# Optimization experiments

Measured on AMD Instinct MI355X. Metric: run time of the kernel, lower is better.

The kernel has to match this reference:

```python
import jax, jax.numpy as jnp
import numpy as np

N = 262144      # active voxels
K = 27          # 3^3 kernel offsets
C_IN = 64
C_OUT = 64
EPS = 1e-5      # BatchNorm eps (torch default)


def setup_inputs() -> dict:
    key = jax.random.key(0)
    k1, k2, k3, k4, k5 = jax.random.split(key, 5)
    features = jax.random.normal(k1, (N, C_IN), dtype=jnp.float32)
    # kernel map: for each offset k and output point i, index of the input
    # neighbor; value == N means 'no neighbor' (maps to a zero pad row)
    nbr_idx = jax.random.randint(k2, (K, N), 0, N + 1)
    weight = jax.random.normal(k3, (K, C_IN, C_OUT), dtype=jnp.float32) * (1.0 / np.sqrt(K * C_IN))
    gamma = jax.random.uniform(k4, (C_OUT,), dtype=jnp.float32, minval=0.5, maxval=1.5)
    beta = jax.random.normal(k5, (C_OUT,), dtype=jnp.float32) * 0.1
    return {"features": features, "nbr_idx": nbr_idx, "weight": weight,
            "gamma": gamma, "beta": beta}


def reference(features, nbr_idx, weight, gamma, beta):
    # zero pad row so idx == N contributes nothing (missing neighbor)
    padded = jnp.concatenate(
        [features, jnp.zeros((1, features.shape[1]), features.dtype)], axis=0)

    def body(acc, kw):
        idx, w = kw                      # idx: [N], w: [C_in, C_out]
        gathered = padded[idx]           # [N, C_in] irregular gather
        return acc + gathered @ w, None  # GEMM + scatter-accumulate

    acc0 = jnp.zeros((features.shape[0], weight.shape[2]), features.dtype)
    out, _ = jax.lax.scan(body, acc0, (nbr_idx, weight))  # [N, C_out]

    # BatchNorm1d over points (training-mode batch statistics)
    mean = jnp.mean(out, axis=0)
    var = jnp.var(out, axis=0)
    out = (out - mean) * jax.lax.rsqrt(var + EPS) * gamma + beta
    # ReLU
    return jnp.maximum(out, 0.0)
```

## Files before the change

kernel.cpp:

```cpp
#include <hip/hip_runtime.h>
#include <hip/hip_bf16.h>
#include <stdint.h>

#define N_PTS 262144
#define KOFF 27
#define CIN 64
#define COUT 64
#define EPS 1e-5f

typedef __attribute__((ext_vector_type(8))) short short8;
typedef __attribute__((ext_vector_type(4))) float f32x4;
typedef __attribute__((ext_vector_type(4))) unsigned short ushort4v;

typedef __attribute__((address_space(3))) unsigned int lds_u32;
typedef __attribute__((address_space(1))) const unsigned int glb_u32;
#define GLDS16(g, s) __builtin_amdgcn_global_load_lds((glb_u32*)(g), (lds_u32*)(s), 16, 0, 0)

static __device__ __forceinline__ unsigned short f32_to_bf16(float f) {
    union { float f; unsigned int u; } v; v.f = f;
    unsigned int u = v.u;
    unsigned int rounded = u + 0x7FFF + ((u >> 16) & 1);
    return (unsigned short)(rounded >> 16);
}

__global__ void k_packW(const float* __restrict__ w, unsigned short* __restrict__ pw) {
    int tid = blockIdx.x * blockDim.x + threadIdx.x;
    if (tid >= KOFF * 4096) return;
    int e = tid & 7;
    int l = (tid >> 3) & 63;
    int t = (tid >> 9) & 3;
    int s = (tid >> 11) & 1;
    int k = tid >> 12;
    int cin  = s * 32 + (l >> 4) * 8 + e;
    int cout = t * 16 + (l & 15);
    pw[tid] = f32_to_bf16(w[(k * CIN + cin) * COUT + cout]);
}

__global__ void k_feat2bf16(const float* __restrict__ feat, unsigned short* __restrict__ out) {
    int gid = blockIdx.x * blockDim.x + threadIdx.x;
    const int total4 = (N_PTS + 1) * CIN / 4;
    if (gid >= total4) return;
    int base = gid * 4;
    ushort4v o;
    if (base < N_PTS * CIN) {
        f32x4 f = *reinterpret_cast<const f32x4*>(feat + base);
        o[0] = f32_to_bf16(f[0]); o[1] = f32_to_bf16(f[1]);
        o[2] = f32_to_bf16(f[2]); o[3] = f32_to_bf16(f[3]);
    } else {
        o[0] = 0; o[1] = 0; o[2] = 0; o[3] = 0;
    }
    *reinterpret_cast<ushort4v*>(out + base) = o;
}

__global__ __launch_bounds__(256, 3) void k_conv(
    const unsigned short* __restrict__ feat,
    const int* __restrict__ nbr,
    const unsigned short* __restrict__ pw,
    float* __restrict__ conv_out,
    float* __restrict__ grp)
{
    __shared__ short8 ldsB[3][512];

    const int tid = threadIdx.x;
    const int l  = tid & 63;
    const int w  = tid >> 6;
    const int lr = l & 15;
    const int lg = l >> 4;
    const int rowbase = blockIdx.x * 128 + w * 32;
    const int r0 = rowbase + lr;
    const int r1 = r0 + 16;
    const int lane_cin = lg * 8;

    f32x4 acc[2][4] = {};
    const short8* pwv = reinterpret_cast<const short8*>(pw);

    int   idxr[3][2];
    short8 a[3][4];

    idxr[0][0] = nbr[r0];          idxr[0][1] = nbr[r1];
    idxr[1][0] = nbr[N_PTS + r0];  idxr[1][1] = nbr[N_PTS + r1];
    idxr[2][0] = nbr[2 * N_PTS + r0]; idxr[2][1] = nbr[2 * N_PTS + r1];
    {
        const short8* g0 = reinterpret_cast<const short8*>(feat + (long)idxr[0][0] * 64 + lane_cin);
        const short8* g1 = reinterpret_cast<const short8*>(feat + (long)idxr[0][1] * 64 + lane_cin);
        a[0][0] = g0[0]; a[0][1] = g0[4]; a[0][2] = g1[0]; a[0][3] = g1[4];
    }
    idxr[0][0] = nbr[3 * N_PTS + r0]; idxr[0][1] = nbr[3 * N_PTS + r1];
    GLDS16(pwv + w * 128 + l,      &ldsB[0][w * 128]);
    GLDS16(pwv + w * 128 + 64 + l, &ldsB[0][w * 128 + 64]);
    {
        const short8* g0 = reinterpret_cast<const short8*>(feat + (long)idxr[1][0] * 64 + lane_cin);
        const short8* g1 = reinterpret_cast<const short8*>(feat + (long)idxr[1][1] * 64 + lane_cin);
        a[1][0] = g0[0]; a[1][1] = g0[4]; a[1][2] = g1[0]; a[1][3] = g1[4];
    }

#define STEP(JV, P0, P1, P2) do {                                              \
        const int j_ = (JV);                                                   \
        const int kI = (j_ + 2 <= KOFF - 1) ? j_ + 2 : KOFF - 1;               \
        idxr[P2][0] = nbr[kI * N_PTS + r0];                                    \
        idxr[P2][1] = nbr[kI * N_PTS + r1];                                    \
        const int kB = (j_ - 1 <= KOFF - 1) ? j_ - 1 : KOFF - 1;               \
        GLDS16(pwv + kB * 512 + w * 128 + l,      &ldsB[P2][w * 128]);         \
        GLDS16(pwv + kB * 512 + w * 128 + 64 + l, &ldsB[P2][w * 128 + 64]);    \
        {                                                                      \
            const short8* g0 = reinterpret_cast<const short8*>(feat + (long)idxr[P0][0] * 64 + lane_cin); \
            const short8* g1 = reinterpret_cast<const short8*>(feat + (long)idxr[P0][1] * 64 + lane_cin); \
            a[P0][0] = g0[0]; a[P0][1] = g0[4];                                \
            a[P0][2] = g1[0]; a[P0][3] = g1[4];                                \
        }                                                                      \
        asm volatile("s_waitcnt vmcnt(12)" ::: "memory");                      \
        __builtin_amdgcn_s_barrier();                                          \
        {                                                                      \
            const short8* cb = &ldsB[P1][0];                                   \
            short8 b0 = cb[l];       short8 b1 = cb[64 + l];                   \
            short8 b2 = cb[128 + l]; short8 b3 = cb[192 + l];                  \
            short8 b4 = cb[256 + l]; short8 b5 = cb[320 + l];                  \
            short8 b6 = cb[384 + l]; short8 b7 = cb[448 + l];                  \
            acc[0][0] = __builtin_amdgcn_mfma_f32_16x16x32_bf16(a[P1][0], b0, acc[0][0], 0, 0, 0); \
            acc[1][0] = __builtin_amdgcn_mfma_f32_16x16x32_bf16(a[P1][2], b0, acc[1][0], 0, 0, 0); \
            acc[0][1] = __builtin_amdgcn_mfma_f32_16x16x32_bf16(a[P1][0], b1, acc[0][1], 0, 0, 0); \
            acc[1][1] = __builtin_amdgcn_mfma_f32_16x16x32_bf16(a[P1][2], b1, acc[1][1], 0, 0, 0); \
            acc[0][2] = __builtin_amdgcn_mfma_f32_16x16x32_bf16(a[P1][0], b2, acc[0][2], 0, 0, 0); \
            acc[1][2] = __builtin_amdgcn_mfma_f32_16x16x32_bf16(a[P1][2], b2, acc[1][2], 0, 0, 0); \
            acc[0][3] = __builtin_amdgcn_mfma_f32_16x16x32_bf16(a[P1][0], b3, acc[0][3], 0, 0, 0); \
            acc[1][3] = __builtin_amdgcn_mfma_f32_16x16x32_bf16(a[P1][2], b3, acc[1][3], 0, 0, 0); \
            acc[0][0] = __builtin_amdgcn_mfma_f32_16x16x32_bf16(a[P1][1], b4, acc[0][0], 0, 0, 0); \
            acc[1][0] = __builtin_amdgcn_mfma_f32_16x16x32_bf16(a[P1][3], b4, acc[1][0], 0, 0, 0); \
            acc[0][1] = __builtin_amdgcn_mfma_f32_16x16x32_bf16(a[P1][1], b5, acc[0][1], 0, 0, 0); \
            acc[1][1] = __builtin_amdgcn_mfma_f32_16x16x32_bf16(a[P1][3], b5, acc[1][1], 0, 0, 0); \
            acc[0][2] = __builtin_amdgcn_mfma_f32_16x16x32_bf16(a[P1][1], b6, acc[0][2], 0, 0, 0); \
            acc[1][2] = __builtin_amdgcn_mfma_f32_16x16x32_bf16(a[P1][3], b6, acc[1][2], 0, 0, 0); \
            acc[0][3] = __builtin_amdgcn_mfma_f32_16x16x32_bf16(a[P1][1], b7, acc[0][3], 0, 0, 0); \
            acc[1][3] = __builtin_amdgcn_mfma_f32_16x16x32_bf16(a[P1][3], b7, acc[1][3], 0, 0, 0); \
        }                                                                      \
    } while (0)

    for (int jt = 0; jt < 9; ++jt) {
        const int j = 2 + jt * 3;
        STEP(j,     2, 0, 1);
        STEP(j + 1, 0, 1, 2);
        STEP(j + 2, 1, 2, 0);
    }
#undef STEP

    const int orow_base = rowbase + lg * 4;
    float psum[4], psq[4];
    #pragma unroll
    for (int t = 0; t < 4; ++t) {
        const int c = t * 16 + lr;
        float s = 0.f, q = 0.f;
        #pragma unroll
        for (int m = 0; m < 2; ++m) {
            #pragma unroll
            for (int e = 0; e < 4; ++e) {
                float v = acc[m][t][e];
                conv_out[(orow_base + m * 16 + e) * 64 + c] = v;
                s += v; q += v * v;
            }
        }
        psum[t] = s; psq[t] = q;
    }
    #pragma unroll
    for (int t = 0; t < 4; ++t) {
        psum[t] += __shfl_xor(psum[t], 16, 64);
        psum[t] += __shfl_xor(psum[t], 32, 64);
        psq[t]  += __shfl_xor(psq[t],  16, 64);
        psq[t]  += __shfl_xor(psq[t],  32, 64);
    }
    if (lg == 0) {
        float* g = grp + (blockIdx.x & 63) * 128;
        #pragma unroll
        for (int t = 0; t < 4; ++t) {
            const int c = t * 16 + lr;
            atomicAdd(&g[c],      psum[t]);
            atomicAdd(&g[64 + c], psq[t]);
        }
    }
}

__global__ void k_stats(const float* __restrict__ grp,
                        const float* __restrict__ gamma,
                        const float* __restrict__ beta,
                        float* __restrict__ ss) {
    __shared__ float red[128];
    const int j = threadIdx.x;
    float s = 0.f;
    for (int g = 0; g < 64; ++g) s += grp[g * 128 + j];
    red[j] = s;
    __syncthreads();
    if (j < 64) {
        float mean  = red[j] / (float)N_PTS;
        float var   = red[64 + j] / (float)N_PTS - mean * mean;
        float scale = gamma[j] * rsqrtf(var + EPS);
        ss[j]      = scale;
        ss[64 + j] = beta[j] - mean * scale;
    }
}

__global__ void k_bnrelu(float* __restrict__ out, const float* __restrict__ ss) {
    int gid = blockIdx.x * blockDim.x + threadIdx.x;
    int base = gid * 4;
    int c0 = base & 63;
    f32x4 v  = *reinterpret_cast<f32x4*>(out + base);
    f32x4 sc = *reinterpret_cast<const f32x4*>(ss + c0);
    f32x4 sh = *reinterpret_cast<const f32x4*>(ss + 64 + c0);
    f32x4 r;
    #pragma unroll
    for (int j = 0; j < 4; ++j) r[j] = fmaxf(v[j] * sc[j] + sh[j], 0.f);
    *reinterpret_cast<f32x4*>(out + base) = r;
}

extern "C" void kernel_launch(void* const* d_in, const int* in_sizes, int n_in,
                              void* d_out, int out_size, void* d_ws, size_t ws_size,
                              hipStream_t stream) {
    const float* features = (const float*)d_in[0];
    const int*   nbr      = (const int*)d_in[1];
    const float* weight   = (const float*)d_in[2];
    const float* gamma    = (const float*)d_in[3];
    const float* beta     = (const float*)d_in[4];
    float* out = (float*)d_out;
    char* ws = (char*)d_ws;

    const size_t off_feat = 0;
    const size_t off_pw   = 33554560;
    const size_t off_grp  = off_pw + 221184;
    const size_t off_ss   = off_grp + 32768;
    unsigned short* feat16 = (unsigned short*)(ws + off_feat);
    unsigned short* pw     = (unsigned short*)(ws + off_pw);
    float*          grp    = (float*)(ws + off_grp);
    float*          ss     = (float*)(ws + off_ss);

    hipMemsetAsync(grp, 0, 64 * 128 * sizeof(float), stream);
    k_packW<<<(KOFF * 4096 + 255) / 256, 256, 0, stream>>>(weight, pw);
    k_feat2bf16<<<((N_PTS + 1) * CIN / 4 + 255) / 256, 256, 0, stream>>>(features, feat16);
    k_conv<<<N_PTS / 128, 256, 0, stream>>>(feat16, nbr, pw, out, grp);
    k_stats<<<1, 128, 0, stream>>>(grp, gamma, beta, ss);
    k_bnrelu<<<N_PTS * COUT / 4 / 256, 256, 0, stream>>>(out, ss);
}
```

Baseline: 191.0 us.

## Quantize features to int8 and weights to two-level int8 for i8 MFMA

Features are quantized to int8 with a global absmax scale, and weights are split into a coarse and a residual int8 term. The gathered convolution then runs on i32_16x16x64_i8 MFMAs with two accumulator sets, rescaled to float in the epilogue. This halves the gathered row bytes and the feature conversion traffic, but adds two extra reduction kernels and a global atomic. Using int8 activations with a single tensor-wide scale reduces accuracy compared with bf16 and may exceed the tolerance.

```diff
diff --git a/kernel.cpp b/kernel.cpp
--- a/kernel.cpp
+++ b/kernel.cpp
@@ -4,62 +4,109 @@
 
 #define N_PTS 262144
 #define KOFF 27
-#define CIN 64
-#define COUT 64
 #define EPS 1e-5f
 
-typedef __attribute__((ext_vector_type(8))) short short8;
+typedef __attribute__((ext_vector_type(4))) int   int4v;
 typedef __attribute__((ext_vector_type(4))) float f32x4;
-typedef __attribute__((ext_vector_type(4))) unsigned short ushort4v;
 
 typedef __attribute__((address_space(3))) unsigned int lds_u32;
 typedef __attribute__((address_space(1))) const unsigned int glb_u32;
 #define GLDS16(g, s) __builtin_amdgcn_global_load_lds((glb_u32*)(g), (lds_u32*)(s), 16, 0, 0)
 
-static __device__ __forceinline__ unsigned short f32_to_bf16(float f) {
-    union { float f; unsigned int u; } v; v.f = f;
-    unsigned int u = v.u;
-    unsigned int rounded = u + 0x7FFF + ((u >> 16) & 1);
-    return (unsigned short)(rounded >> 16);
-}
-
-__global__ void k_packW(const float* __restrict__ w, unsigned short* __restrict__ pw) {
-    int tid = blockIdx.x * blockDim.x + threadIdx.x;
-    if (tid >= KOFF * 4096) return;
-    int e = tid & 7;
-    int l = (tid >> 3) & 63;
-    int t = (tid >> 9) & 3;
-    int s = (tid >> 11) & 1;
-    int k = tid >> 12;
-    int cin  = s * 32 + (l >> 4) * 8 + e;
-    int cout = t * 16 + (l & 15);
-    pw[tid] = f32_to_bf16(w[(k * CIN + cin) * COUT + cout]);
-}
-
-__global__ void k_feat2bf16(const float* __restrict__ feat, unsigned short* __restrict__ out) {
+#define MFMA_I8(a, b, c) __builtin_amdgcn_mfma_i32_16x16x64_i8((a), (b), (c), 0, 0, 0)
+
+__global__ void k_absmax(const float* __restrict__ f, unsigned int* __restrict__ amax) {
     int gid = blockIdx.x * blockDim.x + threadIdx.x;
-    const int total4 = (N_PTS + 1) * CIN / 4;
-    if (gid >= total4) return;
-    int base = gid * 4;
-    ushort4v o;
-    if (base < N_PTS * CIN) {
-        f32x4 f = *reinterpret_cast<const f32x4*>(feat + base);
-        o[0] = f32_to_bf16(f[0]); o[1] = f32_to_bf16(f[1]);
-        o[2] = f32_to_bf16(f[2]); o[3] = f32_to_bf16(f[3]);
+    float m = 0.f;
+    const f32x4* v = reinterpret_cast<const f32x4*>(f);
+    for (int i = gid; i < N_PTS * 64 / 4; i += gridDim.x * blockDim.x) {
+        f32x4 x = v[i];
+        m = fmaxf(m, fmaxf(fmaxf(fabsf(x[0]), fabsf(x[1])), fmaxf(fabsf(x[2]), fabsf(x[3]))));
+    }
+    #pragma unroll
+    for (int o = 32; o; o >>= 1) m = fmaxf(m, __shfl_xor(m, o, 64));
+    if ((threadIdx.x & 63) == 0) atomicMax(amax, __float_as_uint(m));
+}
+
+__global__ void k_wmax(const float* __restrict__ w, float* __restrict__ wmax) {
+    __shared__ float red[4];
+    float m = 0.f;
+    for (int i = threadIdx.x; i < KOFF * 64 * 64; i += 256) m = fmaxf(m, fabsf(w[i]));
+    #pragma unroll
+    for (int o = 32; o; o >>= 1) m = fmaxf(m, __shfl_xor(m, o, 64));
+    if ((threadIdx.x & 63) == 0) red[threadIdx.x >> 6] = m;
+    __syncthreads();
+    if (threadIdx.x == 0) *wmax = fmaxf(fmaxf(red[0], red[1]), fmaxf(red[2], red[3]));
+}
+
+__global__ void k_feat2i8(const float* __restrict__ feat,
+                          const unsigned int* __restrict__ amax_u,
+                          char* __restrict__ out) {
+    int gid = blockIdx.x * blockDim.x + threadIdx.x;
+    const int total = (N_PTS + 1) * 64 / 16;
+    if (gid >= total) return;
+    const float inv = 127.0f / __uint_as_float(*amax_u);
+    const int base = gid * 16;
+    int4v o;
+    if (base < N_PTS * 64) {
+        const f32x4* v = reinterpret_cast<const f32x4*>(feat + base);
+        int wd[4];
+        #pragma unroll
+        for (int d = 0; d < 4; ++d) {
+            f32x4 x = v[d];
+            int b0 = (int)fminf(fmaxf(rintf(x[0] * inv), -127.f), 127.f);
+            int b1 = (int)fminf(fmaxf(rintf(x[1] * inv), -127.f), 127.f);
+            int b2 = (int)fminf(fmaxf(rintf(x[2] * inv), -127.f), 127.f);
+            int b3 = (int)fminf(fmaxf(rintf(x[3] * inv), -127.f), 127.f);
+            wd[d] = (b0 & 255) | ((b1 & 255) << 8) | ((b2 & 255) << 16) | ((b3 & 255) << 24);
+        }
+        o[0] = wd[0]; o[1] = wd[1]; o[2] = wd[2]; o[3] = wd[3];
     } else {
         o[0] = 0; o[1] = 0; o[2] = 0; o[3] = 0;
     }
-    *reinterpret_cast<ushort4v*>(out + base) = o;
+    *reinterpret_cast<int4v*>(out + base) = o;
+}
+
+__global__ void k_packWi8(const float* __restrict__ w,
+                          const float* __restrict__ wmaxp,
+                          char* __restrict__ pb) {
+    int tid = blockIdx.x * blockDim.x + threadIdx.x;
+    if (tid >= KOFF * 512) return;
+    const int k = tid >> 9, slot = tid & 511;
+    const int tbl = slot >> 8, rem = slot & 255, t = rem >> 6, l = rem & 63;
+    const int cin0 = (l >> 4) * 16, cout = t * 16 + (l & 15);
+    const float s1 = *wmaxp / 127.0f;
+    const float s2 = s1 * (1.0f / 128.0f);
+    int wd[4];
+    #pragma unroll
+    for (int d = 0; d < 4; ++d) {
+        int bytes[4];
+        #pragma unroll
+        for (int e4 = 0; e4 < 4; ++e4) {
+            const int e = d * 4 + e4;
+            float wv = w[(k * 64 + cin0 + e) * 64 + cout];
+            float q1 = fminf(fmaxf(rintf(wv / s1), -127.f), 127.f);
+            float r  = wv - q1 * s1;
+            float q2 = fminf(fmaxf(rintf(r / s2), -127.f), 127.f);
+            bytes[e4] = (int)(tbl ? q2 : q1);
+        }
+        wd[d] = (bytes[0] & 255) | ((bytes[1] & 255) << 8) |
+                ((bytes[2] & 255) << 16) | ((bytes[3] & 255) << 24);
+    }
+    int4v o; o[0] = wd[0]; o[1] = wd[1]; o[2] = wd[2]; o[3] = wd[3];
+    *reinterpret_cast<int4v*>(pb + tid * 16) = o;
 }
 
 __global__ __launch_bounds__(256, 3) void k_conv(
-    const unsigned short* __restrict__ feat,
+    const char* __restrict__ fi8,
     const int* __restrict__ nbr,
-    const unsigned short* __restrict__ pw,
+    const char* __restrict__ pb,
     float* __restrict__ conv_out,
-    float* __restrict__ grp)
+    float* __restrict__ grp,
+    const unsigned int* __restrict__ amax_u,
+    const float* __restrict__ wmaxp)
 {
-    __shared__ short8 ldsB[3][512];
+    __shared__ int4v ldsB[3][512];
 
     const int tid = threadIdx.x;
     const int l  = tid & 63;
@@ -69,69 +116,64 @@
     const int rowbase = blockIdx.x * 128 + w * 32;
     const int r0 = rowbase + lr;
     const int r1 = r0 + 16;
-    const int lane_cin = lg * 8;
-
-    f32x4 acc[2][4] = {};
-    const short8* pwv = reinterpret_cast<const short8*>(pw);
+    const int coff = lg * 16;
+
+    int4v zero; zero[0] = 0; zero[1] = 0; zero[2] = 0; zero[3] = 0;
+    int4v acc1[2][4], acc2[2][4];
+    #pragma unroll
+    for (int m = 0; m < 2; ++m)
+        #pragma unroll
+        for (int t = 0; t < 4; ++t) { acc1[m][t] = zero; acc2[m][t] = zero; }
+
+    const int4v* pbv = reinterpret_cast<const int4v*>(pb);
+    const volatile int* vnbr = nbr;
 
     int   idxr[3][2];
-    short8 a[3][4];
-
-    idxr[0][0] = nbr[r0];          idxr[0][1] = nbr[r1];
-    idxr[1][0] = nbr[N_PTS + r0];  idxr[1][1] = nbr[N_PTS + r1];
-    idxr[2][0] = nbr[2 * N_PTS + r0]; idxr[2][1] = nbr[2 * N_PTS + r1];
+    int4v a[3][2];
+
+    idxr[0][0] = vnbr[r0];              idxr[0][1] = vnbr[r1];
+    idxr[1][0] = vnbr[N_PTS + r0];      idxr[1][1] = vnbr[N_PTS + r1];
+    idxr[2][0] = vnbr[2 * N_PTS + r0];  idxr[2][1] = vnbr[2 * N_PTS + r1];
     {
-        const short8* g0 = reinterpret_cast<const short8*>(feat + (long)idxr[0][0] * 64 + lane_cin);
-        const short8* g1 = reinterpret_cast<const short8*>(feat + (long)idxr[0][1] * 64 + lane_cin);
-        a[0][0] = g0[0]; a[0][1] = g0[4]; a[0][2] = g1[0]; a[0][3] = g1[4];
-    }
-    idxr[0][0] = nbr[3 * N_PTS + r0]; idxr[0][1] = nbr[3 * N_PTS + r1];
-    GLDS16(pwv + w * 128 + l,      &ldsB[0][w * 128]);
-    GLDS16(pwv + w * 128 + 64 + l, &ldsB[0][w * 128 + 64]);
+        const int4v* g0 = reinterpret_cast<const int4v*>(fi8 + (long)idxr[0][0] * 64 + coff);
+        const int4v* g1 = reinterpret_cast<const int4v*>(fi8 + (long)idxr[0][1] * 64 + coff);
+        a[0][0] = g0[0]; a[0][1] = g1[0];
+    }
+    idxr[0][0] = vnbr[3 * N_PTS + r0];  idxr[0][1] = vnbr[3 * N_PTS + r1];
+    GLDS16(pbv + w * 64 + l,       &ldsB[0][w * 64]);
+    GLDS16(pbv + 256 + w * 64 + l, &ldsB[0][256 + w * 64]);
     {
-        const short8* g0 = reinterpret_cast<const short8*>(feat + (long)idxr[1][0] * 64 + lane_cin);
-        const short8* g1 = reinterpret_cast<const short8*>(feat + (long)idxr[1][1] * 64 + lane_cin);
-        a[1][0] = g0[0]; a[1][1] = g0[4]; a[1][2] = g1[0]; a[1][3] = g1[4];
+        const int4v* g0 = reinterpret_cast<const int4v*>(fi8 + (long)idxr[1][0] * 64 + coff);
+        const int4v* g1 = reinterpret_cast<const int4v*>(fi8 + (long)idxr[1][1] * 64 + coff);
+        a[1][0] = g0[0]; a[1][1] = g1[0];
     }
 
 #define STEP(JV, P0, P1, P2) do {                                              \
         const int j_ = (JV);                                                   \
-        const int kI = (j_ + 2 <= KOFF - 1) ? j_ + 2 : KOFF - 1;               \
-        idxr[P2][0] = nbr[kI * N_PTS + r0];                                    \
-        idxr[P2][1] = nbr[kI * N_PTS + r1];                                    \
+        const int kI = (j_ + 2) % KOFF;                                        \
+        idxr[P2][0] = vnbr[kI * N_PTS + r0];                                   \
+        idxr[P2][1] = vnbr[kI * N_PTS + r1];                                   \
         const int kB = (j_ - 1 <= KOFF - 1) ? j_ - 1 : KOFF - 1;               \
-        GLDS16(pwv + kB * 512 + w * 128 + l,      &ldsB[P2][w * 128]);         \
-        GLDS16(pwv + kB * 512 + w * 128 + 64 + l, &ldsB[P2][w * 128 + 64]);    \
+        GLDS16(pbv + kB * 512 + w * 64 + l,       &ldsB[P2][w * 64]);          \
+        GLDS16(pbv + kB * 512 + 256 + w * 64 + l, &ldsB[P2][256 + w * 64]);    \
         {                                                                      \
-            const short8* g0 = reinterpret_cast<const short8*>(feat + (long)idxr[P0][0] * 64 + lane_cin); \
-            const short8* g1 = reinterpret_cast<const short8*>(feat + (long)idxr[P0][1] * 64 + lane_cin); \
-            a[P0][0] = g0[0]; a[P0][1] = g0[4];                                \
-            a[P0][2] = g1[0]; a[P0][3] = g1[4];                                \
+            const int4v* g0 = reinterpret_cast<const int4v*>(fi8 + (long)idxr[P0][0] * 64 + coff); \
+            const int4v* g1 = reinterpret_cast<const int4v*>(fi8 + (long)idxr[P0][1] * 64 + coff); \
+            a[P0][0] = g0[0]; a[P0][1] = g1[0];                                \
         }                                                                      \
-        asm volatile("s_waitcnt vmcnt(12)" ::: "memory");                      \
+        asm volatile("s_waitcnt vmcnt(6)" ::: "memory");                       \
         __builtin_amdgcn_s_barrier();                                          \
         {                                                                      \
-            const short8* cb = &ldsB[P1][0];                                   \
-            short8 b0 = cb[l];       short8 b1 = cb[64 + l];                   \
-            short8 b2 = cb[128 + l]; short8 b3 = cb[192 + l];                  \
-            short8 b4 = cb[256 + l]; short8 b5 = cb[320 + l];                  \
-            short8 b6 = cb[384 + l]; short8 b7 = cb[448 + l];                  \
-            acc[0][0] = __builtin_amdgcn_mfma_f32_16x16x32_bf16(a[P1][0], b0, acc[0][0], 0, 0, 0); \
-            acc[1][0] = __builtin_amdgcn_mfma_f32_16x16x32_bf16(a[P1][2], b0, acc[1][0], 0, 0, 0); \
-            acc[0][1] = __builtin_amdgcn_mfma_f32_16x16x32_bf16(a[P1][0], b1, acc[0][1], 0, 0, 0); \
-            acc[1][1] = __builtin_amdgcn_mfma_f32_16x16x32_bf16(a[P1][2], b1, acc[1][1], 0, 0, 0); \
-            acc[0][2] = __builtin_amdgcn_mfma_f32_16x16x32_bf16(a[P1][0], b2, acc[0][2], 0, 0, 0); \
-            acc[1][2] = __builtin_amdgcn_mfma_f32_16x16x32_bf16(a[P1][2], b2, acc[1][2], 0, 0, 0); \
-            acc[0][3] = __builtin_amdgcn_mfma_f32_16x16x32_bf16(a[P1][0], b3, acc[0][3], 0, 0, 0); \
-            acc[1][3] = __builtin_amdgcn_mfma_f32_16x16x32_bf16(a[P1][2], b3, acc[1][3], 0, 0, 0); \
-            acc[0][0] = __builtin_amdgcn_mfma_f32_16x16x32_bf16(a[P1][1], b4, acc[0][0], 0, 0, 0); \
-            acc[1][0] = __builtin_amdgcn_mfma_f32_16x16x32_bf16(a[P1][3], b4, acc[1][0], 0, 0, 0); \
-            acc[0][1] = __builtin_amdgcn_mfma_f32_16x16x32_bf16(a[P1][1], b5, acc[0][1], 0, 0, 0); \
-            acc[1][1] = __builtin_amdgcn_mfma_f32_16x16x32_bf16(a[P1][3], b5, acc[1][1], 0, 0, 0); \
-            acc[0][2] = __builtin_amdgcn_mfma_f32_16x16x32_bf16(a[P1][1], b6, acc[0][2], 0, 0, 0); \
-            acc[1][2] = __builtin_amdgcn_mfma_f32_16x16x32_bf16(a[P1][3], b6, acc[1][2], 0, 0, 0); \
-            acc[0][3] = __builtin_amdgcn_mfma_f32_16x16x32_bf16(a[P1][1], b7, acc[0][3], 0, 0, 0); \
-            acc[1][3] = __builtin_amdgcn_mfma_f32_16x16x32_bf16(a[P1][3], b7, acc[1][3], 0, 0, 0); \
+            const int4v* cb = &ldsB[P1][0];                                    \
+            int4v b;                                                           \
+            b = cb[l];           acc1[0][0] = MFMA_I8(a[P1][0], b, acc1[0][0]); acc1[1][0] = MFMA_I8(a[P1][1], b, acc1[1][0]); \
+            b = cb[64 + l];      acc1[0][1] = MFMA_I8(a[P1][0], b, acc1[0][1]); acc1[1][1] = MFMA_I8(a[P1][1], b, acc1[1][1]); \
+            b = cb[128 + l];     acc1[0][2] = MFMA_I8(a[P1][0], b, acc1[0][2]); acc1[1][2] = MFMA_I8(a[P1][1], b, acc1[1][2]); \
+            b = cb[192 + l];     acc1[0][3] = MFMA_I8(a[P1][0], b, acc1[0][3]); acc1[1][3] = MFMA_I8(a[P1][1], b, acc1[1][3]); \
+            b = cb[256 + l];     acc2[0][0] = MFMA_I8(a[P1][0], b, acc2[0][0]); acc2[1][0] = MFMA_I8(a[P1][1], b, acc2[1][0]); \
+            b = cb[320 + l];     acc2[0][1] = MFMA_I8(a[P1][0], b, acc2[0][1]); acc2[1][1] = MFMA_I8(a[P1][1], b, acc2[1][1]); \
+            b = cb[384 + l];     acc2[0][2] = MFMA_I8(a[P1][0], b, acc2[0][2]); acc2[1][2] = MFMA_I8(a[P1][1], b, acc2[1][2]); \
+            b = cb[448 + l];     acc2[0][3] = MFMA_I8(a[P1][0], b, acc2[0][3]); acc2[1][3] = MFMA_I8(a[P1][1], b, acc2[1][3]); \
         }                                                                      \
     } while (0)
 
@@ -143,6 +185,11 @@
     }
 #undef STEP
 
+    const float sa = __uint_as_float(*amax_u) * (1.0f / 127.0f);
+    const float s1 = *wmaxp * (1.0f / 127.0f);
+    const float d1 = sa * s1;
+    const float d2 = d1 * (1.0f / 128.0f);
+
     const int orow_base = rowbase + lg * 4;
     float psum[4], psq[4];
     #pragma unroll
@@ -153,7 +200,7 @@
         for (int m = 0; m < 2; ++m) {
             #pragma unroll
             for (int e = 0; e < 4; ++e) {
-                float v = acc[m][t][e];
+                float v = (float)acc1[m][t][e] * d1 + (float)acc2[m][t][e] * d2;
                 conv_out[(orow_base + m * 16 + e) * 64 + c] = v;
                 s += v; q += v * v;
             }
@@ -221,19 +268,25 @@
     float* out = (float*)d_out;
     char* ws = (char*)d_ws;
 
-    const size_t off_feat = 0;
-    const size_t off_pw   = 33554560;
-    const size_t off_grp  = off_pw + 221184;
-    const size_t off_ss   = off_grp + 32768;
-    unsigned short* feat16 = (unsigned short*)(ws + off_feat);
-    unsigned short* pw     = (unsigned short*)(ws + off_pw);
-    float*          grp    = (float*)(ws + off_grp);
-    float*          ss     = (float*)(ws + off_ss);
-
-    hipMemsetAsync(grp, 0, 64 * 128 * sizeof(float), stream);
-    k_packW<<<(KOFF * 4096 + 255) / 256, 256, 0, stream>>>(weight, pw);
-    k_feat2bf16<<<((N_PTS + 1) * CIN / 4 + 255) / 256, 256, 0, stream>>>(features, feat16);
-    k_conv<<<N_PTS / 128, 256, 0, stream>>>(feat16, nbr, pw, out, grp);
-    k_stats<<<1, 128, 0, stream>>>(grp, gamma, beta, ss);
-    k_bnrelu<<<N_PTS * COUT / 4 / 256, 256, 0, stream>>>(out, ss);
-}
+    const size_t off_fi8 = 0;
+    const size_t off_pb  = 16777344;
+    const size_t off_grp = off_pb + 221184;
+    const size_t off_sc  = off_grp + 32768;
+    const size_t off_ss  = off_sc + 16;
+    char*         fi8    = ws + off_fi8;
+    char*         pbuf   = ws + off_pb;
+    float*        grp    = (float*)(ws + off_grp);
+    unsigned int* amax   = (unsigned int*)(ws + off_sc);
+    float*        wmax   = (float*)(ws + off_sc) + 1;
+    float*        ss     = (float*)(ws + off_ss);
+
+    hipMemsetAsync(ws + off_grp, 0, 32768 + 16, stream);
+
+    k_absmax <<<2048, 256, 0, stream>>>(features, amax);
+    k_wmax   <<<1,    256, 0, stream>>>(weight, wmax);
+    k_feat2i8<<<((N_PTS + 1) * 64 / 16 + 255) / 256, 256, 0, stream>>>(features, amax, fi8);
+    k_packWi8<<<(KOFF * 512 + 255) / 256, 256, 0, stream>>>(weight, wmax, pbuf);
+    k_conv   <<<N_PTS / 128, 256, 0, stream>>>(fi8, nbr, pbuf, out, grp, amax, wmax);
+    k_stats  <<<1, 128, 0, stream>>>(grp, gamma, beta, ss);
+    k_bnrelu <<<N_PTS * 64 / 4 / 256, 256, 0, stream>>>(out, ss);
+}
```

Result: slower. 343.5 us (+79.8%).
